# Performance work log

Measured on AMD Instinct MI355X. Metric: run time of the kernel, lower is better.

The kernel has to match this reference:

```python
import jax, jax.numpy as jnp
import numpy as np

B, S, D, H, BLEN, FF = 4, 4096, 1024, 16, 256, 4096
DH = D // H
NEG = -1e9
EPS = 1e-6


def setup_inputs() -> dict:
    key = jax.random.key(0)
    ks = jax.random.split(key, 8)
    s = 0.02
    return {
        "X": jax.random.normal(ks[0], (B, S, D), jnp.float32),
        "Wq": jax.random.normal(ks[1], (D, D), jnp.float32) * s,
        "Wk": jax.random.normal(ks[2], (D, D), jnp.float32) * s,
        "Wv": jax.random.normal(ks[3], (D, D), jnp.float32) * s,
        "Wo": jax.random.normal(ks[4], (D, D), jnp.float32) * s,
        "g_attn": jnp.ones((D,), jnp.float32),
        "b_attn": jnp.zeros((D,), jnp.float32),
        "W1": jax.random.normal(ks[5], (D, FF), jnp.float32) * s,
        "b1": jnp.zeros((FF,), jnp.float32),
        "W2": jax.random.normal(ks[6], (FF, D), jnp.float32) * s,
        "b2": jnp.zeros((D,), jnp.float32),
        "g_ffn": jnp.ones((D,), jnp.float32),
        "b_ffn": jnp.zeros((D,), jnp.float32),
    }


def _layernorm(x, g, b):
    mu = jnp.mean(x, axis=-1, keepdims=True)
    var = jnp.mean(jnp.square(x - mu), axis=-1, keepdims=True)
    return (x - mu) * jax.lax.rsqrt(var + EPS) * g + b


def _local_attn(X, Wq, Wk, Wv, Wo):
    def split_heads(y):  # [B,S,D] -> [B,H,S,DH]
        return y.reshape(B, S, H, DH).transpose(0, 2, 1, 3)

    q = split_heads(X @ Wq) * (DH ** -0.5)
    k = split_heads(X @ Wk)
    v = split_heads(X @ Wv)

    nb = S // BLEN  # S is a multiple of BLEN, so the torch pad is a no-op
    q = q.reshape(B, H, nb, BLEN, DH)
    k = k.reshape(B, H, nb, BLEN, DH)
    v = v.reshape(B, H, nb, BLEN, DH)

    # First block: plain causal attention within block 0.
    causal = NEG * jnp.triu(jnp.ones((BLEN, BLEN), jnp.float32), 1)
    logits0 = jnp.einsum('bhkd,bhqd->bhqk', k[:, :, 0], q[:, :, 0]) + causal
    out0 = jax.nn.softmax(logits0, axis=-1) @ v[:, :, 0]  # [B,H,BLEN,DH]

    # Tail blocks attend to [previous block, current block].
    local_k = jnp.concatenate([k[:, :, :-1], k[:, :, 1:]], axis=3)  # [B,H,nb-1,2B,DH]
    local_v = jnp.concatenate([v[:, :, :-1], v[:, :, 1:]], axis=3)
    tail_q = q[:, :, 1:]
    bias = NEG * jnp.triu(jnp.ones((BLEN, 2 * BLEN), jnp.float32), BLEN + 1)
    logits = jnp.einsum('bhnkd,bhnqd->bhnqk', local_k, tail_q) + bias
    tail = jnp.einsum('bhnqk,bhnkd->bhnqd', jax.nn.softmax(logits, axis=-1), local_v)
    tail = tail.reshape(B, H, S - BLEN, DH)

    res = jnp.concatenate([out0, tail], axis=2)       # [B,H,S,DH]
    res = res.transpose(0, 2, 1, 3).reshape(B, S, D)  # merge heads
    return res @ Wo


def reference(X, Wq, Wk, Wv, Wo, g_attn, b_attn, W1, b1, W2, b2, g_ffn, b_ffn):
    y = _local_attn(X, Wq, Wk, Wv, Wo)
    X = _layernorm(y + X, g_attn, b_attn)
    y = jax.nn.relu(X @ W1 + b1) @ W2 + b2
    X = _layernorm(y + X, g_ffn, b_ffn)
    return X
```

## Files before the change

### kernel.cpp

```cpp
#include <hip/hip_runtime.h>
#include <stdint.h>

#define B_    4
#define S_    4096
#define D_    1024
#define H_    16
#define DH_   64
#define BLEN_ 256
#define FF_   4096
#define M_    16384

typedef unsigned short u16;
typedef __attribute__((ext_vector_type(8))) short s8v;
typedef __attribute__((ext_vector_type(4))) short s4v;
typedef __attribute__((ext_vector_type(4))) float f4v;

#define MFMA32(A,B,C) __builtin_amdgcn_mfma_f32_16x16x32_bf16(A,B,C,0,0,0)
#define BAR() asm volatile("s_barrier" ::: "memory")

__device__ __forceinline__ f4v mfma16(s4v a, s4v b, f4v c) {
#if defined(__HIP_DEVICE_COMPILE__)
#if __has_builtin(__builtin_amdgcn_mfma_f32_16x16x16bf16_1k)
  return __builtin_amdgcn_mfma_f32_16x16x16bf16_1k(a, b, c, 0, 0, 0);
#elif __has_builtin(__builtin_amdgcn_mfma_f32_16x16x16_bf16_1k)
  return __builtin_amdgcn_mfma_f32_16x16x16_bf16_1k(a, b, c, 0, 0, 0);
#elif __has_builtin(__builtin_amdgcn_mfma_f32_16x16x16_bf16)
  return __builtin_amdgcn_mfma_f32_16x16x16_bf16(a, b, c, 0, 0, 0);
#else
  f4v d;
  asm volatile("v_mfma_f32_16x16x16_bf16 %0, %1, %2, %3"
               : "=v"(d) : "v"(a), "v"(b), "v"(c));
  return d;
#endif
#else
  (void)a; (void)b; return c;
#endif
}

__device__ __forceinline__ u16 f2b(float f) {
  union { float f; unsigned u; } v; v.f = f;
  unsigned r = v.u + 0x7fffu + ((v.u >> 16) & 1u);
  return (u16)(r >> 16);
}
__device__ __forceinline__ float b2f(u16 h) {
  union { unsigned u; float f; } v; v.u = ((unsigned)h) << 16; return v.f;
}

__device__ __forceinline__ void gld16(const void* gp, void* lp) {
  __builtin_amdgcn_global_load_lds(
      (const __attribute__((address_space(1))) void*)(uintptr_t)gp,
      (__attribute__((address_space(3))) void*)(uintptr_t)lp, 16, 0, 0);
}


__global__ __launch_bounds__(256) void k_castx(const float* __restrict__ in, u16* __restrict__ out) {
  long i = (long)blockIdx.x * 256 + threadIdx.x;
  float4 v = ((const float4*)in)[i];
  s4v o; o[0] = (short)f2b(v.x); o[1] = (short)f2b(v.y);
  o[2] = (short)f2b(v.z); o[3] = (short)f2b(v.w);
  *(s4v*)(out + i * 4) = o;
}

__global__ __launch_bounds__(256) void k_wt(const float* __restrict__ in, u16* __restrict__ out,
                                            int K, int N, float scale) {
  __shared__ u16 tile[32][33];
  const int tx = threadIdx.x & 31, ty = threadIdx.x >> 5;
  const int kb = blockIdx.y << 5, nb = blockIdx.x << 5;
#pragma unroll
  for (int r = 0; r < 4; r++) {
    int row = ty + r * 8;
    tile[row][tx] = f2b(in[(long)(kb + row) * N + nb + tx] * scale);
  }
  __syncthreads();
#pragma unroll
  for (int r = 0; r < 4; r++) {
    int row = ty + r * 8;
    out[(long)(nb + row) * K + kb + tx] = tile[tx][row];
  }
}

template<int QM, int QN>
__device__ __forceinline__ void phmfma(f4v (&acc)[8][4], s8v (&A)[4][2], s8v (&B)[2][2]) {
#pragma unroll
  for (int mt = 0; mt < 4; mt++)
#pragma unroll
    for (int nt = 0; nt < 2; nt++) {
      acc[QM * 4 + mt][QN * 2 + nt] = MFMA32(A[mt][0], B[nt][0], acc[QM * 4 + mt][QN * 2 + nt]);
      acc[QM * 4 + mt][QN * 2 + nt] = MFMA32(A[mt][1], B[nt][1], acc[QM * 4 + mt][QN * 2 + nt]);
    }
}

#define RD_A(d, half, DST) \
  _Pragma("unroll") for (int mt = 0; mt < 4; mt++) { \
    DST[mt][0] = rdA(d, mt + (half) * 4, 0); DST[mt][1] = rdA(d, mt + (half) * 4, 1); }
#define RD_B(d, half, DST) \
  _Pragma("unroll") for (int nt = 0; nt < 2; nt++) { \
    DST[nt][0] = rdB(d, nt + (half) * 2, 0); DST[nt][1] = rdB(d, nt + (half) * 2, 1); }

#define PHASE(GATE, READS, STAGE, QM, QN, AA, BB) \
  READS STAGE \
  BAR(); \
  asm volatile("s_waitcnt lgkmcnt(0)" ::: "memory"); \
  __builtin_amdgcn_sched_barrier(0); \
  __builtin_amdgcn_s_setprio(1); \
  phmfma<QM, QN>(acc, AA, BB); \
  __builtin_amdgcn_s_setprio(0); \
  asm volatile("s_waitcnt vmcnt(" #GATE ")" ::: "memory"); \
  BAR();

template<int EPI, int K, int NB>
__global__ __launch_bounds__(512, 2) void k_gemm256(
    const u16* __restrict__ A, const u16* __restrict__ Bt,
    const float* __restrict__ bias, const void* __restrict__ res,
    u16* __restrict__ out, int N) {
  __shared__ __align__(16) u16 sA[2][16384];
  __shared__ __align__(16) u16 sB[2][16384];
  const int t = threadIdx.x, lane = t & 63, w = t >> 6;
  const int wm = w >> 2, wn = w & 3;
  const int nwg = gridDim.x, cpx = nwg >> 3, orig = blockIdx.x;
  const int wg = (orig & 7) * cpx + (orig >> 3);
  const int nb = wg % NB, mb = wg / NB;
  const int m0 = mb << 8, n0 = nb << 8;
  constexpr int NT = K >> 6;
  constexpr int NP = NT >> 1;

  const int srow = lane >> 3;
  const int scol = ((lane & 7) ^ srow) << 3;
  const u16* gA = A + (size_t)(m0 + srow) * K + scol;
  const u16* gB = Bt + (size_t)(n0 + srow) * K + scol;

  auto stA = [&](int d, int h, int kt) {
#pragma unroll
    for (int i = 0; i < 2; i++) {
      int c = i * 8 + w;
      gld16(gA + (size_t)(h * 128 + c * 8) * K + kt * 64, &sA[d][h * 8192 + c * 512]);
    }
  };
  auto stB = [&](int d, int h, int kt) {
#pragma unroll
    for (int i = 0; i < 2; i++) {
      int c = i * 8 + w;
      gld16(gB + (size_t)(h * 128 + c * 8) * K + kt * 64, &sB[d][h * 8192 + c * 512]);
    }
  };

  const int swz = (lane & 7) << 4;
  const int g8b = (lane >> 4) << 4;
  const int r16 = lane & 15;
  auto rdA = [&](int d, int mt, int kh) -> s8v {
    int byt = (mt * 32 + wm * 16 + r16) * 128 + ((kh * 64 + g8b) ^ swz);
    return *(const s8v*)((const char*)sA[d] + byt);
  };
  auto rdB = [&](int d, int nt, int kh) -> s8v {
    int byt = (nt * 64 + wn * 16 + r16) * 128 + ((kh * 64 + g8b) ^ swz);
    return *(const s8v*)((const char*)sB[d] + byt);
  };

  f4v acc[8][4];
  f4v zz = {0.f, 0.f, 0.f, 0.f};
#pragma unroll
  for (int i = 0; i < 8; i++)
#pragma unroll
    for (int j = 0; j < 4; j++) acc[i][j] = zz;

  stA(0, 0, 0); stB(0, 0, 0); stB(0, 1, 0); stA(0, 1, 0);
  stA(1, 0, 1); stB(1, 0, 1); stB(1, 1, 1);
  asm volatile("s_waitcnt vmcnt(10)" ::: "memory");
  BAR();

  s8v a0[4][2], a1[4][2], bb0[2][2], bb1[2][2];

  for (int pp = 0; pp < NP - 1; ++pp) {
    const int j = pp * 2;
    PHASE(10, RD_A(0, 0, a0) RD_B(0, 0, bb0), stA(1, 1, j + 1);, 0, 0, a0, bb0)
    PHASE(10, RD_B(0, 1, bb1),                stA(0, 0, j + 2);, 0, 1, a0, bb1)
    PHASE(10, RD_A(0, 1, a1),                 stB(0, 0, j + 2);, 1, 0, a1, bb0)
    PHASE(10, ,                               stB(0, 1, j + 2);, 1, 1, a1, bb1)
    PHASE(10, RD_A(1, 0, a0) RD_B(1, 0, bb0), stA(0, 1, j + 2);, 0, 0, a0, bb0)
    PHASE(10, RD_B(1, 1, bb1),                stA(1, 0, j + 3);, 0, 1, a0, bb1)
    PHASE(10, RD_A(1, 1, a1),                 stB(1, 0, j + 3);, 1, 0, a1, bb0)
    PHASE(10, ,                               stB(1, 1, j + 3);, 1, 1, a1, bb1)
  }
  PHASE(10, RD_A(0, 0, a0) RD_B(0, 0, bb0), stA(1, 1, NT - 1);, 0, 0, a0, bb0)
  PHASE(8,  RD_B(0, 1, bb1),                ,                   0, 1, a0, bb1)
  PHASE(8,  RD_A(0, 1, a1),                 ,                   1, 0, a1, bb0)
  PHASE(4,  ,                               ,                   1, 1, a1, bb1)
  PHASE(2,  RD_A(1, 0, a0) RD_B(1, 0, bb0), ,                   0, 0, a0, bb0)
  PHASE(0,  RD_B(1, 1, bb1),                ,                   0, 1, a0, bb1)
  PHASE(0,  RD_A(1, 1, a1),                 ,                   1, 0, a1, bb0)
  PHASE(0,  ,                               ,                   1, 1, a1, bb1)

  const int g4 = (lane >> 4) << 2;
#pragma unroll
  for (int mt = 0; mt < 8; mt++) {
#pragma unroll
    for (int nt = 0; nt < 4; nt++) {
      const int col = n0 + nt * 64 + wn * 16 + r16;
      const long rbase = m0 + mt * 32 + wm * 16 + g4;
      float bcol = 0.f;
      if constexpr (EPI == 2 || EPI == 3) bcol = bias[col];
#pragma unroll
      for (int r = 0; r < 4; r++) {
        long idx = (rbase + r) * (long)N + col;
        float v = acc[mt][nt][r];
        if constexpr (EPI == 1) v += ((const float*)res)[idx];
        if constexpr (EPI == 2) { v += bcol; v = fmaxf(v, 0.f); }
        if constexpr (EPI == 3) { v += bcol + b2f(((const u16*)res)[idx]); }
        out[idx] = f2b(v);
      }
    }
  }
}

__global__ __launch_bounds__(256) void k_attn(const u16* __restrict__ QKV, u16* __restrict__ Aout) {
  __shared__ __align__(16) u16 sK[64 * 64];
  __shared__ __align__(16) u16 sVT[64 * 64];
  const int t = threadIdx.x, lane = t & 63, w = t >> 6;
  const int qblock = blockIdx.x;
  const int b = blockIdx.y >> 4, h = blockIdx.y & 15;
  const int qcol = lane & 15, g = lane >> 4, g4 = g << 2;
  const int win = (qblock == 0) ? 0 : (qblock - 1) * BLEN_;
  const int nch = (qblock == 0) ? 4 : 8;
  const int qbw = qblock * BLEN_ + w * 64;
  const long rowbase = (long)b * S_;
  const int LDQ = 3072;

  s8v qf[4][2];
#pragma unroll
  for (int nt = 0; nt < 4; nt++)
#pragma unroll
    for (int kh = 0; kh < 2; kh++)
      qf[nt][kh] = *(const s8v*)(QKV + (rowbase + qbw + nt * 16 + qcol) * LDQ + h * DH_ + kh * 32 + (g << 3));

  f4v zz = {0.f, 0.f, 0.f, 0.f};
  f4v acc[4][4];
#pragma unroll
  for (int i = 0; i < 4; i++)
#pragma unroll
    for (int j = 0; j < 4; j++) acc[i][j] = zz;
  float mrow[4] = {-1e30f, -1e30f, -1e30f, -1e30f};
  float lrow[4] = {0.f, 0.f, 0.f, 0.f};

  for (int c = 0; c < nch; ++c) {
    const int kb = win + c * 64;
    __syncthreads();
#pragma unroll
    for (int p = 0; p < 2; p++) {
      int key = p * 32 + (t >> 3);
      int d8 = (t & 7) << 3;
      s8v kv = *(const s8v*)(QKV + (rowbase + kb + key) * LDQ + 1024 + h * DH_ + d8);
      int bo = key * 128 + d8 * 2; bo ^= (key & 7) << 4;
      *(s8v*)((char*)sK + bo) = kv;
    }
#pragma unroll
    for (int p = 0; p < 2; p++) {
      int key = (t & 31) + (p << 5);
      int d8 = (t >> 5) << 3;
      s8v vv = *(const s8v*)(QKV + (rowbase + kb + key) * LDQ + 2048 + h * DH_ + d8);
#pragma unroll
      for (int j = 0; j < 8; j++) {
        int dh = d8 + j;
        int bo = dh * 128 + key * 2; bo ^= (dh & 7) << 3;
        *(u16*)((char*)sVT + bo) = (u16)vv[j];
      }
    }
    __syncthreads();
    if (kb > qbw + 63) continue;

    f4v st[4][4];
#pragma unroll
    for (int i = 0; i < 4; i++)
#pragma unroll
      for (int j = 0; j < 4; j++) st[i][j] = zz;
#pragma unroll
    for (int kh = 0; kh < 2; kh++) {
#pragma unroll
      for (int mt = 0; mt < 4; mt++) {
        int key = mt * 16 + qcol;
        int bo = key * 128 + kh * 64 + (g << 4); bo ^= (key & 7) << 4;
        s8v kf = *(const s8v*)((const char*)sK + bo);
#pragma unroll
        for (int nt = 0; nt < 4; nt++) st[mt][nt] = MFMA32(kf, qf[nt][kh], st[mt][nt]);
      }
    }
    if (kb + 63 > qbw) {
#pragma unroll
      for (int mt = 0; mt < 4; mt++) {
        int kbase = kb + mt * 16 + g4;
#pragma unroll
        for (int nt = 0; nt < 4; nt++) {
          int qabs = qbw + nt * 16 + qcol;
#pragma unroll
          for (int r = 0; r < 4; r++)
            if (kbase + r > qabs) st[mt][nt][r] = -1e30f;
        }
      }
    }
    s4v pf[4][4];
#pragma unroll
    for (int nt = 0; nt < 4; nt++) {
      float cm = -1e30f;
#pragma unroll
      for (int mt = 0; mt < 4; mt++)
#pragma unroll
        for (int r = 0; r < 4; r++) cm = fmaxf(cm, st[mt][nt][r]);
      cm = fmaxf(cm, __shfl_xor(cm, 16));
      cm = fmaxf(cm, __shfl_xor(cm, 32));
      float mnew = fmaxf(mrow[nt], cm);
      float sc = __expf(mrow[nt] - mnew);
      mrow[nt] = mnew;
      float ps = 0.f;
#pragma unroll
      for (int kt = 0; kt < 4; kt++) {
        s4v pp;
#pragma unroll
        for (int r = 0; r < 4; r++) {
          float sv = st[kt][nt][r];
          float p = (sv > -1e29f) ? __expf(sv - mnew) : 0.f;
          ps += p;
          pp[r] = (short)f2b(p);
        }
        pf[nt][kt] = pp;
      }
      ps += __shfl_xor(ps, 16);
      ps += __shfl_xor(ps, 32);
      lrow[nt] = lrow[nt] * sc + ps;
#pragma unroll
      for (int dt = 0; dt < 4; dt++) acc[dt][nt] *= sc;
    }
#pragma unroll
    for (int dt = 0; dt < 4; dt++) {
      int dh = dt * 16 + qcol;
#pragma unroll
      for (int kt = 0; kt < 4; kt++) {
        int bo = dh * 128 + kt * 32 + (g << 3); bo ^= (dh & 7) << 3;
        s4v vf = *(const s4v*)((const char*)sVT + bo);
#pragma unroll
        for (int nt = 0; nt < 4; nt++) acc[dt][nt] = mfma16(vf, pf[nt][kt], acc[dt][nt]);
      }
    }
  }

#pragma unroll
  for (int nt = 0; nt < 4; nt++) {
    float inv = 1.f / lrow[nt];
    long qrow = rowbase + qbw + nt * 16 + qcol;
#pragma unroll
    for (int dt = 0; dt < 4; dt++) {
      s4v o;
#pragma unroll
      for (int r = 0; r < 4; r++) o[r] = (short)f2b(acc[dt][nt][r] * inv);
      *(s4v*)(Aout + qrow * D_ + h * DH_ + dt * 16 + g4) = o;
    }
  }
}

template<int OUTB>
__global__ __launch_bounds__(256) void k_ln(const u16* __restrict__ in, const float* __restrict__ gw,
                                            const float* __restrict__ bw, float* __restrict__ outf,
                                            u16* __restrict__ outb) {
  const int t = threadIdx.x, lane = t & 63, w = t >> 6;
  const long base = (long)blockIdx.x * D_;
  s4v xv = *(const s4v*)(in + base + t * 4);
  float v0 = b2f((u16)xv[0]), v1 = b2f((u16)xv[1]), v2 = b2f((u16)xv[2]), v3 = b2f((u16)xv[3]);
  float s = v0 + v1 + v2 + v3;
  float s2 = v0 * v0 + v1 * v1 + v2 * v2 + v3 * v3;
#pragma unroll
  for (int off = 1; off < 64; off <<= 1) { s += __shfl_xor(s, off); s2 += __shfl_xor(s2, off); }
  __shared__ float red[8];
  if (lane == 0) { red[w] = s; red[4 + w] = s2; }
  __syncthreads();
  s = red[0] + red[1] + red[2] + red[3];
  s2 = red[4] + red[5] + red[6] + red[7];
  float mu = s * (1.f / D_);
  float var = s2 * (1.f / D_) - mu * mu;
  float rstd = rsqrtf(var + 1e-6f);
  float4 gv = ((const float4*)gw)[t];
  float4 bv = ((const float4*)bw)[t];
  float o0 = (v0 - mu) * rstd * gv.x + bv.x;
  float o1 = (v1 - mu) * rstd * gv.y + bv.y;
  float o2 = (v2 - mu) * rstd * gv.z + bv.z;
  float o3 = (v3 - mu) * rstd * gv.w + bv.w;
  if constexpr (OUTB) {
    s4v o; o[0] = (short)f2b(o0); o[1] = (short)f2b(o1); o[2] = (short)f2b(o2); o[3] = (short)f2b(o3);
    *(s4v*)(outb + base + t * 4) = o;
  } else {
    float4 o; o.x = o0; o.y = o1; o.z = o2; o.w = o3;
    *(float4*)(outf + base + t * 4) = o;
  }
}


extern "C" void kernel_launch(void* const* d_in, const int* in_sizes, int n_in,
                              void* d_out, int out_size, void* d_ws, size_t ws_size,
                              hipStream_t stream) {
  const float* X      = (const float*)d_in[0];
  const float* Wq     = (const float*)d_in[1];
  const float* Wk     = (const float*)d_in[2];
  const float* Wv     = (const float*)d_in[3];
  const float* Wo     = (const float*)d_in[4];
  const float* g_attn = (const float*)d_in[5];
  const float* b_attn = (const float*)d_in[6];
  const float* W1     = (const float*)d_in[7];
  const float* b1     = (const float*)d_in[8];
  const float* W2     = (const float*)d_in[9];
  const float* b2     = (const float*)d_in[10];
  const float* g_ffn  = (const float*)d_in[11];
  const float* b_ffn  = (const float*)d_in[12];
  float* out = (float*)d_out;

  char* ws = (char*)d_ws;
  const size_t MB = 1ull << 20;
  u16* WqkvT = (u16*)(ws + 0 * MB);
  u16* WoT   = (u16*)(ws + 6 * MB);
  u16* W1T   = (u16*)(ws + 8 * MB);
  u16* W2T   = (u16*)(ws + 16 * MB);
  u16* Xb    = (u16*)(ws + 24 * MB);
  u16* QKVb  = (u16*)(ws + 56 * MB);
  u16* Ab    = (u16*)(ws + 152 * MB);
  u16* Yb    = (u16*)(ws + 184 * MB);
  u16* Mid   = QKVb;

  dim3 b256(256), b512(512);
  k_wt<<<dim3(32, 32),  b256, 0, stream>>>(Wq, WqkvT,               1024, 1024, 0.125f);
  k_wt<<<dim3(32, 32),  b256, 0, stream>>>(Wk, WqkvT + 1024 * 1024, 1024, 1024, 1.0f);
  k_wt<<<dim3(32, 32),  b256, 0, stream>>>(Wv, WqkvT + 2048 * 1024, 1024, 1024, 1.0f);
  k_wt<<<dim3(32, 32),  b256, 0, stream>>>(Wo, WoT, 1024, 1024, 1.0f);
  k_wt<<<dim3(128, 32), b256, 0, stream>>>(W1, W1T, 1024, 4096, 1.0f);
  k_wt<<<dim3(32, 128), b256, 0, stream>>>(W2, W2T, 4096, 1024, 1.0f);
  k_castx<<<dim3(16384), b256, 0, stream>>>(X, Xb);

  k_gemm256<0, 1024, 12><<<dim3(768), b512, 0, stream>>>(Xb, WqkvT, nullptr, nullptr, QKVb, 3072);
  k_attn<<<dim3(16, B_ * H_), b256, 0, stream>>>(QKVb, Ab);
  k_gemm256<1, 1024, 4><<<dim3(256), b512, 0, stream>>>(Ab, WoT, nullptr, X, Yb, 1024);
  k_ln<1><<<dim3(16384), b256, 0, stream>>>(Yb, g_attn, b_attn, nullptr, Xb);
  k_gemm256<2, 1024, 16><<<dim3(1024), b512, 0, stream>>>(Xb, W1T, b1, nullptr, Mid, 4096);
  k_gemm256<3, 4096, 4><<<dim3(256), b512, 0, stream>>>(Mid, W2T, b2, Xb, Yb, 1024);
  k_ln<0><<<dim3(16384), b256, 0, stream>>>(Yb, g_ffn, b_ffn, out, nullptr);

  (void)in_sizes; (void)n_in; (void)out_size; (void)ws_size;
}
```

Baseline: 578.5 us.

## Restructure GEMM main loop into register-prefetched double-buffer pipeline

Replaces the eight-phase barrier-heavy GEMM schedule with a simpler per-k-tile loop. Each iteration issues all global-to-LDS loads for the next tile up front and overlaps LDS reads of the next A/B fragments with MFMA quadrants, using one barrier per tile instead of two per phase. The aim is to cut barrier and waitcnt overhead and overlap LDS reads with MFMAs. In exchange the full vmcnt(0) wait per tile drops the deeper multi-stage global prefetch, and holding all B fragments raises register pressure.

```diff
diff --git a/kernel.cpp b/kernel.cpp
--- a/kernel.cpp
+++ b/kernel.cpp
@@ -17,6 +17,7 @@
 
 #define MFMA32(A,B,C) __builtin_amdgcn_mfma_f32_16x16x32_bf16(A,B,C,0,0,0)
 #define BAR() asm volatile("s_barrier" ::: "memory")
+#define SCHEDB() __builtin_amdgcn_sched_barrier(0)
 
 __device__ __forceinline__ f4v mfma16(s4v a, s4v b, f4v c) {
 #if defined(__HIP_DEVICE_COMPILE__)
@@ -79,35 +80,6 @@
   }
 }
 
-template<int QM, int QN>
-__device__ __forceinline__ void phmfma(f4v (&acc)[8][4], s8v (&A)[4][2], s8v (&B)[2][2]) {
-#pragma unroll
-  for (int mt = 0; mt < 4; mt++)
-#pragma unroll
-    for (int nt = 0; nt < 2; nt++) {
-      acc[QM * 4 + mt][QN * 2 + nt] = MFMA32(A[mt][0], B[nt][0], acc[QM * 4 + mt][QN * 2 + nt]);
-      acc[QM * 4 + mt][QN * 2 + nt] = MFMA32(A[mt][1], B[nt][1], acc[QM * 4 + mt][QN * 2 + nt]);
-    }
-}
-
-#define RD_A(d, half, DST) \
-  _Pragma("unroll") for (int mt = 0; mt < 4; mt++) { \
-    DST[mt][0] = rdA(d, mt + (half) * 4, 0); DST[mt][1] = rdA(d, mt + (half) * 4, 1); }
-#define RD_B(d, half, DST) \
-  _Pragma("unroll") for (int nt = 0; nt < 2; nt++) { \
-    DST[nt][0] = rdB(d, nt + (half) * 2, 0); DST[nt][1] = rdB(d, nt + (half) * 2, 1); }
-
-#define PHASE(GATE, READS, STAGE, QM, QN, AA, BB) \
-  READS STAGE \
-  BAR(); \
-  asm volatile("s_waitcnt lgkmcnt(0)" ::: "memory"); \
-  __builtin_amdgcn_sched_barrier(0); \
-  __builtin_amdgcn_s_setprio(1); \
-  phmfma<QM, QN>(acc, AA, BB); \
-  __builtin_amdgcn_s_setprio(0); \
-  asm volatile("s_waitcnt vmcnt(" #GATE ")" ::: "memory"); \
-  BAR();
-
 template<int EPI, int K, int NB>
 __global__ __launch_bounds__(512, 2) void k_gemm256(
     const u16* __restrict__ A, const u16* __restrict__ Bt,
@@ -122,7 +94,6 @@
   const int nb = wg % NB, mb = wg / NB;
   const int m0 = mb << 8, n0 = nb << 8;
   constexpr int NT = K >> 6;
-  constexpr int NP = NT >> 1;
 
   const int srow = lane >> 3;
   const int scol = ((lane & 7) ^ srow) << 3;
@@ -163,32 +134,69 @@
 #pragma unroll
     for (int j = 0; j < 4; j++) acc[i][j] = zz;
 
-  stA(0, 0, 0); stB(0, 0, 0); stB(0, 1, 0); stA(0, 1, 0);
-  stA(1, 0, 1); stB(1, 0, 1); stB(1, 1, 1);
-  asm volatile("s_waitcnt vmcnt(10)" ::: "memory");
+  stA(0, 0, 0); stA(0, 1, 0); stB(0, 0, 0); stB(0, 1, 0);
+  asm volatile("s_waitcnt vmcnt(0)" ::: "memory");
   BAR();
 
-  s8v a0[4][2], a1[4][2], bb0[2][2], bb1[2][2];
-
-  for (int pp = 0; pp < NP - 1; ++pp) {
-    const int j = pp * 2;
-    PHASE(10, RD_A(0, 0, a0) RD_B(0, 0, bb0), stA(1, 1, j + 1);, 0, 0, a0, bb0)
-    PHASE(10, RD_B(0, 1, bb1),                stA(0, 0, j + 2);, 0, 1, a0, bb1)
-    PHASE(10, RD_A(0, 1, a1),                 stB(0, 0, j + 2);, 1, 0, a1, bb0)
-    PHASE(10, ,                               stB(0, 1, j + 2);, 1, 1, a1, bb1)
-    PHASE(10, RD_A(1, 0, a0) RD_B(1, 0, bb0), stA(0, 1, j + 2);, 0, 0, a0, bb0)
-    PHASE(10, RD_B(1, 1, bb1),                stA(1, 0, j + 3);, 0, 1, a0, bb1)
-    PHASE(10, RD_A(1, 1, a1),                 stB(1, 0, j + 3);, 1, 0, a1, bb0)
-    PHASE(10, ,                               stB(1, 1, j + 3);, 1, 1, a1, bb1)
-  }
-  PHASE(10, RD_A(0, 0, a0) RD_B(0, 0, bb0), stA(1, 1, NT - 1);, 0, 0, a0, bb0)
-  PHASE(8,  RD_B(0, 1, bb1),                ,                   0, 1, a0, bb1)
-  PHASE(8,  RD_A(0, 1, a1),                 ,                   1, 0, a1, bb0)
-  PHASE(4,  ,                               ,                   1, 1, a1, bb1)
-  PHASE(2,  RD_A(1, 0, a0) RD_B(1, 0, bb0), ,                   0, 0, a0, bb0)
-  PHASE(0,  RD_B(1, 1, bb1),                ,                   0, 1, a0, bb1)
-  PHASE(0,  RD_A(1, 1, a1),                 ,                   1, 0, a1, bb0)
-  PHASE(0,  ,                               ,                   1, 1, a1, bb1)
+  s8v a0[4][2], a1[4][2], bb[4][2];
+#pragma unroll
+  for (int m = 0; m < 4; m++) { a0[m][0] = rdA(0, m, 0); a0[m][1] = rdA(0, m, 1); }
+#pragma unroll
+  for (int n = 0; n < 4; n++) { bb[n][0] = rdB(0, n, 0); bb[n][1] = rdB(0, n, 1); }
+  SCHEDB();
+
+  for (int j = 0; j < NT; ++j) {
+    const int d = j & 1, nd = d ^ 1;
+    const bool s1 = (j + 1 < NT);
+
+    if (s1) { stA(nd, 0, j + 1); stA(nd, 1, j + 1); stB(nd, 0, j + 1); stB(nd, 1, j + 1); }
+#pragma unroll
+    for (int m = 0; m < 4; m++) { a1[m][0] = rdA(d, m + 4, 0); a1[m][1] = rdA(d, m + 4, 1); }
+    SCHEDB();
+    __builtin_amdgcn_s_setprio(1);
+#pragma unroll
+    for (int m = 0; m < 4; m++)
+#pragma unroll
+      for (int n = 0; n < 4; n++) {
+        acc[m][n] = MFMA32(a0[m][0], bb[n][0], acc[m][n]);
+        acc[m][n] = MFMA32(a0[m][1], bb[n][1], acc[m][n]);
+      }
+    __builtin_amdgcn_s_setprio(0);
+    SCHEDB();
+    asm volatile("s_waitcnt lgkmcnt(0)" ::: "memory");
+    if (s1) asm volatile("s_waitcnt vmcnt(0)" ::: "memory");
+    BAR();
+    __builtin_amdgcn_s_setprio(1);
+#pragma unroll
+    for (int m = 0; m < 4; m++)
+#pragma unroll
+      for (int n = 0; n < 2; n++) {
+        acc[m + 4][n] = MFMA32(a1[m][0], bb[n][0], acc[m + 4][n]);
+        acc[m + 4][n] = MFMA32(a1[m][1], bb[n][1], acc[m + 4][n]);
+      }
+    __builtin_amdgcn_s_setprio(0);
+    SCHEDB();
+    if (s1) {
+#pragma unroll
+      for (int m = 0; m < 4; m++) { a0[m][0] = rdA(nd, m, 0); a0[m][1] = rdA(nd, m, 1); }
+    }
+    SCHEDB();
+    __builtin_amdgcn_s_setprio(1);
+#pragma unroll
+    for (int m = 0; m < 4; m++)
+#pragma unroll
+      for (int n = 0; n < 2; n++) {
+        acc[m + 4][n + 2] = MFMA32(a1[m][0], bb[n + 2][0], acc[m + 4][n + 2]);
+        acc[m + 4][n + 2] = MFMA32(a1[m][1], bb[n + 2][1], acc[m + 4][n + 2]);
+      }
+    __builtin_amdgcn_s_setprio(0);
+    SCHEDB();
+    if (s1) {
+#pragma unroll
+      for (int n = 0; n < 4; n++) { bb[n][0] = rdB(nd, n, 0); bb[n][1] = rdB(nd, n, 1); }
+    }
+    SCHEDB();
+  }
 
   const int g4 = (lane >> 4) << 2;
 #pragma unroll
```

Measured after the change: 603.1 us. +4.2%, slower.

## Double-buffer attention K/V staging and merge weight transposes into one launch

Applied to the files above, without the earlier changes.

The attention kernel now uses two LDS buffers for K and V^T and issues the global loads for the next chunk before computing on the current one. This cuts the loop from two barriers per chunk to one and lets load latency overlap with MFMA work. Separately, the six weight-transpose launches are folded into a single kernel that looks up its job from a block-offset table, removing five launches. The cost is double the attention LDS footprint (32 KB), which could lower occupancy, plus extra registers held across the compute.

```diff
diff --git a/kernel.cpp b/kernel.cpp
--- a/kernel.cpp
+++ b/kernel.cpp
@@ -61,20 +61,37 @@
   *(s4v*)(out + i * 4) = o;
 }
 
-__global__ __launch_bounds__(256) void k_wt(const float* __restrict__ in, u16* __restrict__ out,
-                                            int K, int N, float scale) {
+struct WtJobs {
+  const float* src[6];
+  u16* dst[6];
+  int K[6];
+  int N[6];
+  float sc[6];
+  int off[7];
+};
+__global__ __launch_bounds__(256) void k_wtall(WtJobs J) {
   __shared__ u16 tile[32][33];
+  const int b = blockIdx.x;
+  int j = 0;
+#pragma unroll
+  for (int q = 0; q < 5; q++) if (b >= J.off[q + 1]) j = q + 1;
+  const float* in = J.src[j];
+  u16* out = J.dst[j];
+  const int K = J.K[j], N = J.N[j];
+  const float scale = J.sc[j];
+  const int r = b - J.off[j];
+  const int nb32 = N >> 5;
+  const int kb = (r / nb32) << 5, nb = (r % nb32) << 5;
   const int tx = threadIdx.x & 31, ty = threadIdx.x >> 5;
-  const int kb = blockIdx.y << 5, nb = blockIdx.x << 5;
-#pragma unroll
-  for (int r = 0; r < 4; r++) {
-    int row = ty + r * 8;
+#pragma unroll
+  for (int rr = 0; rr < 4; rr++) {
+    int row = ty + rr * 8;
     tile[row][tx] = f2b(in[(long)(kb + row) * N + nb + tx] * scale);
   }
   __syncthreads();
 #pragma unroll
-  for (int r = 0; r < 4; r++) {
-    int row = ty + r * 8;
+  for (int rr = 0; rr < 4; rr++) {
+    int row = ty + rr * 8;
     out[(long)(nb + row) * K + kb + tx] = tile[tx][row];
   }
 }
@@ -213,8 +230,8 @@
 }
 
 __global__ __launch_bounds__(256) void k_attn(const u16* __restrict__ QKV, u16* __restrict__ Aout) {
-  __shared__ __align__(16) u16 sK[64 * 64];
-  __shared__ __align__(16) u16 sVT[64 * 64];
+  __shared__ __align__(16) u16 sK[2][64 * 64];
+  __shared__ __align__(16) u16 sVT[2][64 * 64];
   const int t = threadIdx.x, lane = t & 63, w = t >> 6;
   const int qblock = blockIdx.x;
   const int b = blockIdx.y >> 4, h = blockIdx.y & 15;
@@ -225,6 +242,30 @@
   const long rowbase = (long)b * S_;
   const int LDQ = 3072;
 
+  auto stage = [&](int c, int buf) {
+    const int kb2 = win + c * 64;
+#pragma unroll
+    for (int p = 0; p < 2; p++) {
+      int key = p * 32 + (t >> 3);
+      int d8 = (t & 7) << 3;
+      s8v kv = *(const s8v*)(QKV + (rowbase + kb2 + key) * LDQ + 1024 + h * DH_ + d8);
+      int bo = key * 128 + d8 * 2; bo ^= (key & 7) << 4;
+      *(s8v*)((char*)sK[buf] + bo) = kv;
+    }
+#pragma unroll
+    for (int p = 0; p < 2; p++) {
+      int key = (t & 31) + (p << 5);
+      int d8 = (t >> 5) << 3;
+      s8v vv = *(const s8v*)(QKV + (rowbase + kb2 + key) * LDQ + 2048 + h * DH_ + d8);
+#pragma unroll
+      for (int jj = 0; jj < 8; jj++) {
+        int dh = d8 + jj;
+        int bo = dh * 128 + key * 2; bo ^= (dh & 7) << 3;
+        *(u16*)((char*)sVT[buf] + bo) = (u16)vv[jj];
+      }
+    }
+  };
+
   s8v qf[4][2];
 #pragma unroll
   for (int nt = 0; nt < 4; nt++)
@@ -241,104 +282,89 @@
   float mrow[4] = {-1e30f, -1e30f, -1e30f, -1e30f};
   float lrow[4] = {0.f, 0.f, 0.f, 0.f};
 
+  stage(0, 0);
+  __syncthreads();
+
   for (int c = 0; c < nch; ++c) {
     const int kb = win + c * 64;
+    const int buf = c & 1;
+    if (c + 1 < nch) stage(c + 1, buf ^ 1);
+
+    if (kb <= qbw + 63) {
+      f4v st[4][4];
+#pragma unroll
+      for (int i = 0; i < 4; i++)
+#pragma unroll
+        for (int j = 0; j < 4; j++) st[i][j] = zz;
+#pragma unroll
+      for (int kh = 0; kh < 2; kh++) {
+#pragma unroll
+        for (int mt = 0; mt < 4; mt++) {
+          int key = mt * 16 + qcol;
+          int bo = key * 128 + kh * 64 + (g << 4); bo ^= (key & 7) << 4;
+          s8v kf = *(const s8v*)((const char*)sK[buf] + bo);
+#pragma unroll
+          for (int nt = 0; nt < 4; nt++) st[mt][nt] = MFMA32(kf, qf[nt][kh], st[mt][nt]);
+        }
+      }
+      if (kb + 63 > qbw) {
+#pragma unroll
+        for (int mt = 0; mt < 4; mt++) {
+          int kbase = kb + mt * 16 + g4;
+#pragma unroll
+          for (int nt = 0; nt < 4; nt++) {
+            int qabs = qbw + nt * 16 + qcol;
+#pragma unroll
+            for (int r = 0; r < 4; r++)
+              if (kbase + r > qabs) st[mt][nt][r] = -1e30f;
+          }
+        }
+      }
+      s4v pf[4][4];
+#pragma unroll
+      for (int nt = 0; nt < 4; nt++) {
+        float cm = -1e30f;
+#pragma unroll
+        for (int mt = 0; mt < 4; mt++)
+#pragma unroll
+          for (int r = 0; r < 4; r++) cm = fmaxf(cm, st[mt][nt][r]);
+        cm = fmaxf(cm, __shfl_xor(cm, 16));
+        cm = fmaxf(cm, __shfl_xor(cm, 32));
+        float mnew = fmaxf(mrow[nt], cm);
+        float sc = __expf(mrow[nt] - mnew);
+        mrow[nt] = mnew;
+        float ps = 0.f;
+#pragma unroll
+        for (int kt = 0; kt < 4; kt++) {
+          s4v pp;
+#pragma unroll
+          for (int r = 0; r < 4; r++) {
+            float sv = st[kt][nt][r];
+            float p = (sv > -1e29f) ? __expf(sv - mnew) : 0.f;
+            ps += p;
+            pp[r] = (short)f2b(p);
+          }
+          pf[nt][kt] = pp;
+        }
+        ps += __shfl_xor(ps, 16);
+        ps += __shfl_xor(ps, 32);
+        lrow[nt] = lrow[nt] * sc + ps;
+#pragma unroll
+        for (int dt = 0; dt < 4; dt++) acc[dt][nt] *= sc;
+      }
+#pragma unroll
+      for (int dt = 0; dt < 4; dt++) {
+        int dh = dt * 16 + qcol;
+#pragma unroll
+        for (int kt = 0; kt < 4; kt++) {
+          int bo = dh * 128 + kt * 32 + (g << 3); bo ^= (dh & 7) << 3;
+          s4v vf = *(const s4v*)((const char*)sVT[buf] + bo);
+#pragma unroll
+          for (int nt = 0; nt < 4; nt++) acc[dt][nt] = mfma16(vf, pf[nt][kt], acc[dt][nt]);
+        }
+      }
+    }
     __syncthreads();
-#pragma unroll
-    for (int p = 0; p < 2; p++) {
-      int key = p * 32 + (t >> 3);
-      int d8 = (t & 7) << 3;
-      s8v kv = *(const s8v*)(QKV + (rowbase + kb + key) * LDQ + 1024 + h * DH_ + d8);
-      int bo = key * 128 + d8 * 2; bo ^= (key & 7) << 4;
-      *(s8v*)((char*)sK + bo) = kv;
-    }
-#pragma unroll
-    for (int p = 0; p < 2; p++) {
-      int key = (t & 31) + (p << 5);
-      int d8 = (t >> 5) << 3;
-      s8v vv = *(const s8v*)(QKV + (rowbase + kb + key) * LDQ + 2048 + h * DH_ + d8);
-#pragma unroll
-      for (int j = 0; j < 8; j++) {
-        int dh = d8 + j;
-        int bo = dh * 128 + key * 2; bo ^= (dh & 7) << 3;
-        *(u16*)((char*)sVT + bo) = (u16)vv[j];
-      }
-    }
-    __syncthreads();
-    if (kb > qbw + 63) continue;
-
-    f4v st[4][4];
-#pragma unroll
-    for (int i = 0; i < 4; i++)
-#pragma unroll
-      for (int j = 0; j < 4; j++) st[i][j] = zz;
-#pragma unroll
-    for (int kh = 0; kh < 2; kh++) {
-#pragma unroll
-      for (int mt = 0; mt < 4; mt++) {
-        int key = mt * 16 + qcol;
-        int bo = key * 128 + kh * 64 + (g << 4); bo ^= (key & 7) << 4;
-        s8v kf = *(const s8v*)((const char*)sK + bo);
-#pragma unroll
-        for (int nt = 0; nt < 4; nt++) st[mt][nt] = MFMA32(kf, qf[nt][kh], st[mt][nt]);
-      }
-    }
-    if (kb + 63 > qbw) {
-#pragma unroll
-      for (int mt = 0; mt < 4; mt++) {
-        int kbase = kb + mt * 16 + g4;
-#pragma unroll
-        for (int nt = 0; nt < 4; nt++) {
-          int qabs = qbw + nt * 16 + qcol;
-#pragma unroll
-          for (int r = 0; r < 4; r++)
-            if (kbase + r > qabs) st[mt][nt][r] = -1e30f;
-        }
-      }
-    }
-    s4v pf[4][4];
-#pragma unroll
-    for (int nt = 0; nt < 4; nt++) {
-      float cm = -1e30f;
-#pragma unroll
-      for (int mt = 0; mt < 4; mt++)
-#pragma unroll
-        for (int r = 0; r < 4; r++) cm = fmaxf(cm, st[mt][nt][r]);
-      cm = fmaxf(cm, __shfl_xor(cm, 16));
-      cm = fmaxf(cm, __shfl_xor(cm, 32));
-      float mnew = fmaxf(mrow[nt], cm);
-      float sc = __expf(mrow[nt] - mnew);
-      mrow[nt] = mnew;
-      float ps = 0.f;
-#pragma unroll
-      for (int kt = 0; kt < 4; kt++) {
-        s4v pp;
-#pragma unroll
-        for (int r = 0; r < 4; r++) {
-          float sv = st[kt][nt][r];
-          float p = (sv > -1e29f) ? __expf(sv - mnew) : 0.f;
-          ps += p;
-          pp[r] = (short)f2b(p);
-        }
-        pf[nt][kt] = pp;
-      }
-      ps += __shfl_xor(ps, 16);
-      ps += __shfl_xor(ps, 32);
-      lrow[nt] = lrow[nt] * sc + ps;
-#pragma unroll
-      for (int dt = 0; dt < 4; dt++) acc[dt][nt] *= sc;
-    }
-#pragma unroll
-    for (int dt = 0; dt < 4; dt++) {
-      int dh = dt * 16 + qcol;
-#pragma unroll
-      for (int kt = 0; kt < 4; kt++) {
-        int bo = dh * 128 + kt * 32 + (g << 3); bo ^= (dh & 7) << 3;
-        s4v vf = *(const s4v*)((const char*)sVT + bo);
-#pragma unroll
-        for (int nt = 0; nt < 4; nt++) acc[dt][nt] = mfma16(vf, pf[nt][kt], acc[dt][nt]);
-      }
-    }
   }
 
 #pragma unroll
@@ -422,12 +448,17 @@
   u16* Mid   = QKVb;
 
   dim3 b256(256), b512(512);
-  k_wt<<<dim3(32, 32),  b256, 0, stream>>>(Wq, WqkvT,               1024, 1024, 0.125f);
-  k_wt<<<dim3(32, 32),  b256, 0, stream>>>(Wk, WqkvT + 1024 * 1024, 1024, 1024, 1.0f);
-  k_wt<<<dim3(32, 32),  b256, 0, stream>>>(Wv, WqkvT + 2048 * 1024, 1024, 1024, 1.0f);
-  k_wt<<<dim3(32, 32),  b256, 0, stream>>>(Wo, WoT, 1024, 1024, 1.0f);
-  k_wt<<<dim3(128, 32), b256, 0, stream>>>(W1, W1T, 1024, 4096, 1.0f);
-  k_wt<<<dim3(32, 128), b256, 0, stream>>>(W2, W2T, 4096, 1024, 1.0f);
+
+  WtJobs J;
+  J.src[0] = Wq; J.src[1] = Wk; J.src[2] = Wv; J.src[3] = Wo; J.src[4] = W1; J.src[5] = W2;
+  J.dst[0] = WqkvT; J.dst[1] = WqkvT + 1024 * 1024; J.dst[2] = WqkvT + 2048 * 1024;
+  J.dst[3] = WoT; J.dst[4] = W1T; J.dst[5] = W2T;
+  J.K[0] = 1024; J.K[1] = 1024; J.K[2] = 1024; J.K[3] = 1024; J.K[4] = 1024; J.K[5] = 4096;
+  J.N[0] = 1024; J.N[1] = 1024; J.N[2] = 1024; J.N[3] = 1024; J.N[4] = 4096; J.N[5] = 1024;
+  J.sc[0] = 0.125f; J.sc[1] = 1.f; J.sc[2] = 1.f; J.sc[3] = 1.f; J.sc[4] = 1.f; J.sc[5] = 1.f;
+  J.off[0] = 0; J.off[1] = 1024; J.off[2] = 2048; J.off[3] = 3072;
+  J.off[4] = 4096; J.off[5] = 8192; J.off[6] = 12288;
+  k_wtall<<<dim3(12288), b256, 0, stream>>>(J);
   k_castx<<<dim3(16384), b256, 0, stream>>>(X, Xb);
 
   k_gemm256<0, 1024, 12><<<dim3(768), b512, 0, stream>>>(Xb, WqkvT, nullptr, nullptr, QKVb, 3072);
```

New measurement: 597.4 us. +3.3%, slower.
